# Performance work log

Hardware: AMD Instinct MI355X
Metric: run time of the kernel (lower is better)

Reference implementation:

```python
import jax, jax.numpy as jnp
import numpy as np

EPS = 1e-6
NUM_HEADS = 16  # config.num_attention_heads

def _rms(h, w):
    h32 = h.astype(jnp.float32)
    v = jnp.mean(h32 * h32, axis=-1, keepdims=True)
    return (w * h32 * jax.lax.rsqrt(v + EPS)).astype(h.dtype)

def _rope(q, k, pos):
    dh = q.shape[-1]
    inv = 1.0 / (10000.0 ** (jnp.arange(0, dh, 2, dtype=jnp.float32) / dh))
    ang = pos.astype(jnp.float32)[:, None] * inv[None, :]  # [n, dh/2]
    cos = jnp.concatenate([jnp.cos(ang), jnp.cos(ang)], -1)[None, None]  # [1,1,n,dh]
    sin = jnp.concatenate([jnp.sin(ang), jnp.sin(ang)], -1)[None, None]
    def rot(x):
        x1, x2 = x[..., :dh // 2], x[..., dh // 2:]
        return jnp.concatenate([-x2, x1], -1)
    return q * cos + rot(q) * sin, k * cos + rot(k) * sin

def _skip_causal_mask(N, block_size, len1, text_len):
    qi = jnp.arange(N)[:, None]
    ki = jnp.arange(N)[None, :]
    qb = (qi - text_len) // block_size
    kb = (ki - text_len) // block_size
    iq = qi >= text_len
    ik = ki >= text_len
    return (((ki < text_len) & (qi >= ki))
            | (iq & ik & (qb < len1) & (kb < len1) & (qb >= kb))
            | (iq & ik & (qb >= len1) & (kb < len1) & (qb - len1 > kb))
            | (iq & ik & (qb == kb)))

def _layer(x, position_ids, text_position_ids, qkv_w, qkv_b, proj_w, proj_b,
           qn_w, kn_w, ln1_w, ln2_w, gate_w, up_w, down_w,
           block_size, text_len, len1):
    B, N, C = x.shape
    H = NUM_HEADS
    Dh = C // H
    T = text_len
    Lc = len1 * block_size
    offs = [0, T, T + Lc]
    lens = [T, Lc, N - T - Lc]  # text / clean / noised segment lengths
    qs, ks, vs = [], [], []
    for i in range(3):
        seg = _rms(x[:, offs[i]:offs[i] + lens[i]], ln1_w[i])  # input layernorm
        qkv = seg @ qkv_w[i] + qkv_b[i]                        # [B,n,3C]
        qkv = qkv.reshape(B, lens[i], 3, H, Dh).transpose(2, 0, 3, 1, 4)
        qs.append(_rms(qkv[0], qn_w[i]))
        ks.append(_rms(qkv[1], kn_w[i]))
        vs.append(qkv[2])
    img_q = jnp.concatenate([qs[1], qs[2]], axis=2)
    img_k = jnp.concatenate([ks[1], ks[2]], axis=2)
    img_q, img_k = _rope(img_q, img_k, position_ids)
    txt_q, txt_k = _rope(qs[0], ks[0], text_position_ids)
    q = jnp.concatenate([txt_q, img_q], axis=2)
    k = jnp.concatenate([txt_k, img_k], axis=2)
    v = jnp.concatenate(vs, axis=2)
    scores = jnp.einsum('bhqd,bhkd->bhqk', q, k) / np.float32(np.sqrt(Dh))
    mask = _skip_causal_mask(N, block_size, len1, text_len)
    scores = jnp.where(mask, scores, jnp.finfo(scores.dtype).min)
    attn = jax.nn.softmax(scores, axis=-1)
    o = jnp.einsum('bhqk,bhkd->bhqd', attn, v)
    o = o.transpose(0, 2, 1, 3).reshape(B, N, C)
    o = jnp.concatenate([o[:, offs[i]:offs[i] + lens[i]] @ proj_w[i] + proj_b[i]
                         for i in range(3)], axis=1)
    h = x + o
    mlp = []
    for i in range(3):
        y = _rms(h[:, offs[i]:offs[i] + lens[i]], ln2_w[i])  # post-attn layernorm
        mlp.append((jax.nn.silu(y @ gate_w[i]) * (y @ up_w[i])) @ down_w[i])
    return h + jnp.concatenate(mlp, axis=1)

def setup_inputs():
    key = jax.random.key(0)
    ks = jax.random.split(key, 8)
    B, C, H, I = 2, 1024, 16, 4096
    block_size, text_len, len1, len2 = 128, 256, 4, 4
    N = text_len + (len1 + len2) * block_size  # 1280
    s = 0.02
    return {
        'x': jax.random.normal(ks[0], (B, N, C), jnp.float32),
        'position_ids': jnp.arange((len1 + len2) * block_size, dtype=jnp.int32),
        'text_position_ids': jnp.arange(text_len, dtype=jnp.int32),
        'qkv_w': jax.random.normal(ks[1], (3, C, 3 * C), jnp.float32) * s,
        'qkv_b': jnp.zeros((3, 3 * C), jnp.float32),
        'proj_w': jax.random.normal(ks[2], (3, C, C), jnp.float32) * s,
        'proj_b': jnp.zeros((3, C), jnp.float32),
        'qn_w': jnp.ones((3, C // H), jnp.float32),
        'kn_w': jnp.ones((3, C // H), jnp.float32),
        'ln1_w': jnp.ones((3, C), jnp.float32),
        'ln2_w': jnp.ones((3, C), jnp.float32),
        'gate_w': jax.random.normal(ks[3], (3, C, I), jnp.float32) * s,
        'up_w': jax.random.normal(ks[4], (3, C, I), jnp.float32) * s,
        'down_w': jax.random.normal(ks[5], (3, I, C), jnp.float32) * s,
        'block_size': block_size, 'text_len': text_len, 'len1': len1,
    }

def reference(x, position_ids, text_position_ids, qkv_w, qkv_b, proj_w, proj_b,
              qn_w, kn_w, ln1_w, ln2_w, gate_w, up_w, down_w,
              block_size, text_len, len1):
    return _layer(x, position_ids, text_position_ids, qkv_w, qkv_b, proj_w, proj_b,
                  qn_w, kn_w, ln1_w, ln2_w, gate_w, up_w, down_w,
                  block_size, text_len, len1)
```

## Files before the change

### kernel.cpp

```cpp
#include <hip/hip_runtime.h>
#include <math.h>

constexpr int Bb  = 2;
constexpr int Nn  = 1280;
constexpr int Cc  = 1024;
constexpr int Hh  = 16;
constexpr int DH  = 64;
constexpr int Ii  = 4096;
constexpr int Tt  = 256;
constexpr int BSz = 128;
constexpr int L1  = 4;
constexpr int Mrows = Bb * Nn;

typedef __attribute__((ext_vector_type(8))) short short8v;
typedef __attribute__((ext_vector_type(4))) float f32x4;

__device__ __forceinline__ int segof(int n) {
    return n < Tt ? 0 : (n < Tt + L1 * BSz ? 1 : 2);
}
__device__ __forceinline__ unsigned short f2bf(float f) {
    unsigned int u = __float_as_uint(f);
    u += 0x7fffu + ((u >> 16) & 1u);
    return (unsigned short)(u >> 16);
}
__device__ __forceinline__ float bf2f(unsigned short h) {
    return __uint_as_float(((unsigned int)h) << 16);
}

__device__ __forceinline__ int xcd_swz(int lin, int nwg) {
    int cpx = nwg >> 3;
    return (lin & 7) * cpx + (lin >> 3);
}

__device__ __forceinline__ void rms_dev(const float* __restrict__ in,
                                        const float* __restrict__ w,
                                        unsigned short* __restrict__ out,
                                        int row, float* sred) {
    int n   = row % Nn;
    int seg = segof(n);
    const float* x = in + (size_t)row * Cc;
    int t = threadIdx.x;
    float4 xv = reinterpret_cast<const float4*>(x)[t];
    float ss = xv.x * xv.x + xv.y * xv.y + xv.z * xv.z + xv.w * xv.w;
#pragma unroll
    for (int off = 32; off; off >>= 1) ss += __shfl_down(ss, off, 64);
    int lane = t & 63, wid = t >> 6;
    if (lane == 0) sred[wid] = ss;
    __syncthreads();
    if (t == 0) sred[4] = rsqrtf((sred[0] + sred[1] + sred[2] + sred[3]) * (1.0f / Cc) + 1e-6f);
    __syncthreads();
    float r = sred[4];
    float4 wv = reinterpret_cast<const float4*>(w + (size_t)seg * Cc)[t];
    ushort4 ov;
    ov.x = f2bf(wv.x * xv.x * r);
    ov.y = f2bf(wv.y * xv.y * r);
    ov.z = f2bf(wv.z * xv.z * r);
    ov.w = f2bf(wv.w * xv.w * r);
    *reinterpret_cast<ushort4*>(&out[(size_t)row * Cc + t * 4]) = ov;
}

__device__ __forceinline__ void pack_dev(const float* __restrict__ W,
                                         unsigned short* __restrict__ PB,
                                         int K, int Nd, size_t idx) {
    size_t cpseg = (size_t)K * Nd / 8;
    int s = (int)(idx / cpseg);
    size_t rm = idx % cpseg;
    int lane = (int)(rm & 63);
    int fr   = (int)((rm >> 6) & 7);
    size_t tile = rm >> 9;
    int nct = Nd >> 7;
    int cb = (int)(tile % nct);
    int kt = (int)(tile / nct);
    int col = cb * 128 + fr * 16 + (lane & 15);
    int k0  = kt * 32 + (lane >> 4) * 8;
    const float* src = W + ((size_t)s * K + k0) * Nd + col;
    unsigned short o[8];
#pragma unroll
    for (int j = 0; j < 8; j++) o[j] = f2bf(src[(size_t)j * Nd]);
    short8v v;
#pragma unroll
    for (int j = 0; j < 8; j++) v[j] = (short)o[j];
    *reinterpret_cast<short8v*>(&PB[idx * 8]) = v;
}

__global__ __launch_bounds__(256)
void rms_bf16(const float* __restrict__ in, const float* __restrict__ w,
              unsigned short* __restrict__ out) {
    __shared__ float sred[5];
    rms_dev(in, w, out, blockIdx.x, sred);
}

__global__ __launch_bounds__(256)
void pack_w(const float* __restrict__ W, unsigned short* __restrict__ PB,
            int K, int Nd) {
    pack_dev(W, PB, K, Nd, (size_t)blockIdx.x * 256 + threadIdx.x);
}

__global__ __launch_bounds__(256)
void fat1(const float* __restrict__ x, const float* __restrict__ ln1_w,
          unsigned short* __restrict__ xn,
          const float* __restrict__ qkv_w, unsigned short* __restrict__ qkv_p) {
    __shared__ float sred[5];
    int bid = blockIdx.x;
    if (bid < Mrows) {
        rms_dev(x, ln1_w, xn, bid, sred);
    } else {
        pack_dev(qkv_w, qkv_p, Cc, 3 * Cc, (size_t)(bid - Mrows) * 256 + threadIdx.x);
    }
}

__device__ __forceinline__ void attn_dev(
        const unsigned short* __restrict__ Qg, const unsigned short* __restrict__ Kg,
        const unsigned short* __restrict__ Vg, unsigned short* __restrict__ O,
        int qt, int bh,
        unsigned short* k_lds, unsigned short* vt_lds, unsigned short* p_base) {
    int b = bh >> 4, h = bh & 15;
    int tid = threadIdx.x, lane = tid & 63, wid = tid >> 6;
    int g = lane >> 4, c = lane & 15;

    const size_t headoff = (size_t)bh * Nn * DH;
    int q0 = qt * 64;
    bool qtext = q0 < Tt;
    int qb = qtext ? 0 : (q0 - Tt) / BSz;

    int qrow_frag = q0 + wid * 16 + c;
    short8v aq[2];
#pragma unroll
    for (int kb = 0; kb < 2; kb++)
        aq[kb] = *reinterpret_cast<const short8v*>(
            &Qg[headoff + (size_t)qrow_frag * DH + kb * 32 + g * 8]);

    unsigned short* pbuf = p_base + wid * 1024;

    f32x4 o_[4];
#pragma unroll
    for (int nb = 0; nb < 4; nb++) o_[nb] = (f32x4){0.f, 0.f, 0.f, 0.f};
    float m_[4] = {-3.4e38f, -3.4e38f, -3.4e38f, -3.4e38f};
    float l_[4] = {0.f, 0.f, 0.f, 0.f};

    int tr = tid >> 2, tc = tid & 3;

    for (int kt = 0; kt < Nn / 64; kt++) {
        int kbase = kt * 64;
        bool vis, diag = false;
        if (qtext) {
            vis = (kbase <= q0);
            diag = (kbase == q0);
        } else if (kbase < Tt) {
            vis = true;
        } else {
            int kb = (kbase - Tt) / BSz;
            vis = (qb < L1) ? (kb <= qb)
                            : ((kb < L1 && qb - L1 > kb) || kb == qb);
        }
        if (!vis) continue;

        __syncthreads();
        {
            const unsigned short* ks = &Kg[headoff + (size_t)(kbase + tr) * DH];
            const unsigned short* vs = &Vg[headoff + (size_t)(kbase + tr) * DH];
#pragma unroll
            for (int i = 0; i < 2; i++) {
                int ch = tc + i * 4;
                short8v kv = *reinterpret_cast<const short8v*>(ks + ch * 8);
                int byte = (tr * 128 + ch * 16) ^ ((tr & 7) << 4);
                *reinterpret_cast<short8v*>((char*)k_lds + byte) = kv;
                short8v vv = *reinterpret_cast<const short8v*>(vs + ch * 8);
#pragma unroll
                for (int j = 0; j < 8; j++) {
                    int dh = ch * 8 + j;
                    int vbyte = (dh * 128 + tr * 2) ^ ((dh & 7) << 4);
                    *reinterpret_cast<unsigned short*>((char*)vt_lds + vbyte) =
                        (unsigned short)vv[j];
                }
            }
        }
        __syncthreads();

        f32x4 s_[4];
#pragma unroll
        for (int nb = 0; nb < 4; nb++) s_[nb] = (f32x4){0.f, 0.f, 0.f, 0.f};
#pragma unroll
        for (int nb = 0; nb < 4; nb++) {
            int kil = nb * 16 + c;
#pragma unroll
            for (int kb = 0; kb < 2; kb++) {
                int byte = (kil * 128 + kb * 64 + g * 16) ^ ((kil & 7) << 4);
                short8v bk = *reinterpret_cast<short8v*>((char*)k_lds + byte);
                s_[nb] = __builtin_amdgcn_mfma_f32_16x16x32_bf16(aq[kb], bk, s_[nb], 0, 0, 0);
            }
        }
#pragma unroll
        for (int nb = 0; nb < 4; nb++) {
#pragma unroll
            for (int r = 0; r < 4; r++) {
                float sv = s_[nb][r] * 0.125f;
                if (diag) {
                    int qrl = wid * 16 + g * 4 + r;
                    int kcl = nb * 16 + c;
                    if (qrl < kcl) sv = -3.4e38f;
                }
                s_[nb][r] = sv;
            }
        }
#pragma unroll
        for (int r = 0; r < 4; r++) {
            float mx = fmaxf(fmaxf(s_[0][r], s_[1][r]), fmaxf(s_[2][r], s_[3][r]));
#pragma unroll
            for (int off = 1; off <= 8; off <<= 1)
                mx = fmaxf(mx, __shfl_xor(mx, off, 64));
            float mn = fmaxf(m_[r], mx);
            float es = __expf(m_[r] - mn);
            m_[r] = mn;
            float pv[4];
            float rs = 0.f;
#pragma unroll
            for (int nb = 0; nb < 4; nb++) {
                pv[nb] = __expf(s_[nb][r] - mn);
                rs += pv[nb];
            }
#pragma unroll
            for (int off = 1; off <= 8; off <<= 1)
                rs += __shfl_xor(rs, off, 64);
            l_[r] = l_[r] * es + rs;
#pragma unroll
            for (int nb = 0; nb < 4; nb++) o_[nb][r] *= es;
            int qrl = g * 4 + r;
            int swz = (qrl & 7) << 4;
#pragma unroll
            for (int nb = 0; nb < 4; nb++) {
                int byte = (qrl * 128 + (nb * 16 + c) * 2) ^ swz;
                *reinterpret_cast<unsigned short*>((char*)pbuf + byte) = f2bf(pv[nb]);
            }
        }
        short8v aP[2];
#pragma unroll
        for (int kb = 0; kb < 2; kb++) {
            int byte = (c * 128 + kb * 64 + g * 16) ^ ((c & 7) << 4);
            aP[kb] = *reinterpret_cast<short8v*>((char*)pbuf + byte);
        }
#pragma unroll
        for (int nb = 0; nb < 4; nb++) {
            int dh = nb * 16 + c;
#pragma unroll
            for (int kb = 0; kb < 2; kb++) {
                int byte = (dh * 128 + kb * 64 + g * 16) ^ ((dh & 7) << 4);
                short8v bv = *reinterpret_cast<short8v*>((char*)vt_lds + byte);
                o_[nb] = __builtin_amdgcn_mfma_f32_16x16x32_bf16(aP[kb], bv, o_[nb], 0, 0, 0);
            }
        }
    }

    float inv_[4];
#pragma unroll
    for (int r = 0; r < 4; r++) inv_[r] = 1.f / l_[r];
#pragma unroll
    for (int nb = 0; nb < 4; nb++) {
        int col = h * DH + nb * 16 + c;
#pragma unroll
        for (int r = 0; r < 4; r++) {
            int row = q0 + wid * 16 + g * 4 + r;
            O[((size_t)b * Nn + row) * Cc + col] = f2bf(o_[nb][r] * inv_[r]);
        }
    }
}

__global__ __launch_bounds__(256)
void fat2(const unsigned short* __restrict__ Qg, const unsigned short* __restrict__ Kg,
          const unsigned short* __restrict__ Vg, unsigned short* __restrict__ O,
          const float* __restrict__ proj_w, unsigned short* __restrict__ proj_p,
          const float* __restrict__ gate_w, unsigned short* __restrict__ gate_p,
          const float* __restrict__ up_w,   unsigned short* __restrict__ up_p) {
    __shared__ __align__(16) unsigned short k_lds[64 * 64];
    __shared__ __align__(16) unsigned short vt_lds[64 * 64];
    __shared__ __align__(16) unsigned short p_lds[4 * 16 * 64];
    int bid = blockIdx.x;
    if (bid < 640) {
        attn_dev(Qg, Kg, Vg, O, bid % 20, bid / 20, k_lds, vt_lds, p_lds);
        return;
    }
    bid -= 640;
    if (bid < 1536) {
        pack_dev(proj_w, proj_p, Cc, Cc, (size_t)bid * 256 + threadIdx.x);
        return;
    }
    bid -= 1536;
    if (bid < 6144) {
        pack_dev(gate_w, gate_p, Cc, Ii, (size_t)bid * 256 + threadIdx.x);
        return;
    }
    bid -= 6144;
    pack_dev(up_w, up_p, Cc, Ii, (size_t)bid * 256 + threadIdx.x);
}

template <int OUTMODE, bool BIAS, int NZ>
__global__ __launch_bounds__(256, 2)
void gemm128r(const unsigned short* __restrict__ A,
              const unsigned short* __restrict__ PB,
              const float* __restrict__ bias, void* __restrict__ outp,
              int K, int Nd) {
    __shared__ __align__(16) unsigned short lds[8192];
    int bx = blockIdx.x, by = blockIdx.y, bz = (NZ > 1) ? blockIdx.z : 0;
    {
        int gx = gridDim.x, gy = gridDim.y, gz = (NZ > 1) ? gridDim.z : 1;
        int lin = bx + gx * (by + gy * bz);
        int swz = xcd_swz(lin, gx * gy * gz);
        bx = swz % gx; swz /= gx;
        by = swz % gy; bz = swz / gy;
    }
    int rb = bx * 128, cb = by;
    int seg = segof(rb % Nn);
    int tid = threadIdx.x, lane = tid & 63, wid = tid >> 6;
    int wr = wid >> 1, wc = wid & 1;
    int g = lane >> 4, c_ = lane & 15;
    const int nct = Nd >> 7;
    const int Keff = K / NZ;
    const int nKt = Keff >> 5;
    const int kz = bz * Keff;
    const unsigned short* PBseg = PB + (size_t)seg * K * Nd;

    int mf0 = tid >> 6, lc0 = tid & 63;
    const unsigned short* pA0 =
        A + (size_t)(rb + mf0 * 16 + (lc0 & 15)) * K + kz + (lc0 >> 4) * 8;
    const unsigned short* pA1 = pA0 + (size_t)64 * K;
    const unsigned short* pB0 =
        PBseg + (((size_t)(kz >> 5) * nct + cb) * 8 + mf0) * 512 + (size_t)lc0 * 8;
    const unsigned short* pB1 = pB0 + 2048;
    const size_t bstep = (size_t)nct * 4096;

    f32x4 acc[4][4];
#pragma unroll
    for (int m = 0; m < 4; m++)
#pragma unroll
        for (int n = 0; n < 4; n++) acc[m][n] = (f32x4){0.f, 0.f, 0.f, 0.f};

    short8v av[2], bv[2];
    av[0] = *reinterpret_cast<const short8v*>(pA0);
    av[1] = *reinterpret_cast<const short8v*>(pA1);
    bv[0] = *reinterpret_cast<const short8v*>(pB0);
    bv[1] = *reinterpret_cast<const short8v*>(pB1);
    pA0 += 32; pA1 += 32; pB0 += bstep; pB1 += bstep;

    for (int kt = 0; kt < nKt; ++kt) {
        __syncthreads();
        *reinterpret_cast<short8v*>(&lds[(size_t)tid * 8]) = av[0];
        *reinterpret_cast<short8v*>(&lds[(size_t)(tid + 256) * 8]) = av[1];
        *reinterpret_cast<short8v*>(&lds[4096 + (size_t)tid * 8]) = bv[0];
        *reinterpret_cast<short8v*>(&lds[4096 + (size_t)(tid + 256) * 8]) = bv[1];
        __syncthreads();
        if (kt + 1 < nKt) {
            av[0] = *reinterpret_cast<const short8v*>(pA0);
            av[1] = *reinterpret_cast<const short8v*>(pA1);
            bv[0] = *reinterpret_cast<const short8v*>(pB0);
            bv[1] = *reinterpret_cast<const short8v*>(pB1);
            pA0 += 32; pA1 += 32; pB0 += bstep; pB1 += bstep;
        }
        short8v afr[4], bfr[4];
#pragma unroll
        for (int m = 0; m < 4; m++)
            afr[m] = *reinterpret_cast<short8v*>(&lds[((wr * 4 + m) * 64 + lane) * 8]);
#pragma unroll
        for (int n = 0; n < 4; n++)
            bfr[n] = *reinterpret_cast<short8v*>(&lds[4096 + ((wc * 4 + n) * 64 + lane) * 8]);
#pragma unroll
        for (int m = 0; m < 4; m++)
#pragma unroll
            for (int n = 0; n < 4; n++)
                acc[m][n] = __builtin_amdgcn_mfma_f32_16x16x32_bf16(
                    afr[m], bfr[n], acc[m][n], 0, 0, 0);
    }

    float* outf = (float*)outp;
    unsigned short* outh = (unsigned short*)outp;
    size_t zoff = (NZ > 1) ? (size_t)bz * Mrows * Nd : 0;
#pragma unroll
    for (int n = 0; n < 4; n++) {
        int col = cb * 128 + wc * 64 + n * 16 + c_;
        float bvv = BIAS ? bias[(size_t)seg * Nd + col] : 0.f;
#pragma unroll
        for (int m = 0; m < 4; m++) {
#pragma unroll
            for (int r = 0; r < 4; r++) {
                int row = rb + wr * 64 + m * 16 + g * 4 + r;
                float v = acc[m][n][r] + bvv;
                if (OUTMODE == 0) outf[zoff + (size_t)row * Nd + col] = v;
                else              outh[zoff + (size_t)row * Nd + col] = f2bf(v);
            }
        }
    }
}

__global__ __launch_bounds__(256)
void gemm_gu(const unsigned short* __restrict__ A,
             const unsigned short* __restrict__ PG,
             const unsigned short* __restrict__ PU,
             unsigned short* __restrict__ outp) {
    __shared__ __align__(16) unsigned short lds[10240];
    int bx = blockIdx.x, by = blockIdx.y;
    {
        int lin = bx + gridDim.x * by;
        int swz = xcd_swz(lin, gridDim.x * gridDim.y);
        bx = swz % gridDim.x; by = swz / gridDim.x;
    }
    int rb = bx * 64, cb = by;
    int seg = segof(rb % Nn);
    int tid = threadIdx.x, lane = tid & 63, wid = tid >> 6;
    int wr = wid >> 1, wc = wid & 1;
    int g = lane >> 4, c_ = lane & 15;
    const int nct = Ii >> 7;
    const unsigned short* PGseg = PG + (size_t)seg * Cc * Ii;
    const unsigned short* PUseg = PU + (size_t)seg * Cc * Ii;

    f32x4 accG[2][4], accU[2][4];
#pragma unroll
    for (int m = 0; m < 2; m++)
#pragma unroll
        for (int n = 0; n < 4; n++) {
            accG[m][n] = (f32x4){0.f, 0.f, 0.f, 0.f};
            accU[m][n] = (f32x4){0.f, 0.f, 0.f, 0.f};
        }

    int mf0 = tid >> 6, lc0 = tid & 63;
    const unsigned short* gA =
        &A[(size_t)(rb + mf0 * 16 + (lc0 & 15)) * Cc + (lc0 >> 4) * 8];
    short8v av, gv[2], uv[2];
    auto load_tile = [&](int kt) {
        av = *reinterpret_cast<const short8v*>(gA + kt * 32);
#pragma unroll
        for (int i = 0; i < 2; i++) {
            int c = tid + i * 256;
            int cf = c >> 6, lc = c & 63;
            size_t off = (((size_t)kt * nct + cb) * 8 + cf) * 64 * 8 + (size_t)lc * 8;
            gv[i] = *reinterpret_cast<const short8v*>(PGseg + off);
            uv[i] = *reinterpret_cast<const short8v*>(PUseg + off);
        }
    };

    const int nKt = Cc >> 5;
    load_tile(0);
    for (int kt = 0; kt < nKt; ++kt) {
        __syncthreads();
        *reinterpret_cast<short8v*>(&lds[(size_t)tid * 8]) = av;
#pragma unroll
        for (int i = 0; i < 2; i++) {
            *reinterpret_cast<short8v*>(&lds[2048 + (size_t)(tid + i * 256) * 8]) = gv[i];
            *reinterpret_cast<short8v*>(&lds[6144 + (size_t)(tid + i * 256) * 8]) = uv[i];
        }
        __syncthreads();
        if (kt + 1 < nKt) load_tile(kt + 1);
        short8v afr[2], gfr[4], ufr[4];
#pragma unroll
        for (int m = 0; m < 2; m++)
            afr[m] = *reinterpret_cast<short8v*>(&lds[((wr * 2 + m) * 64 + lane) * 8]);
#pragma unroll
        for (int n = 0; n < 4; n++) {
            gfr[n] = *reinterpret_cast<short8v*>(&lds[2048 + ((wc * 4 + n) * 64 + lane) * 8]);
            ufr[n] = *reinterpret_cast<short8v*>(&lds[6144 + ((wc * 4 + n) * 64 + lane) * 8]);
        }
#pragma unroll
        for (int m = 0; m < 2; m++)
#pragma unroll
            for (int n = 0; n < 4; n++) {
                accG[m][n] = __builtin_amdgcn_mfma_f32_16x16x32_bf16(
                    afr[m], gfr[n], accG[m][n], 0, 0, 0);
                accU[m][n] = __builtin_amdgcn_mfma_f32_16x16x32_bf16(
                    afr[m], ufr[n], accU[m][n], 0, 0, 0);
            }
    }

#pragma unroll
    for (int n = 0; n < 4; n++) {
        int col = cb * 128 + wc * 64 + n * 16 + c_;
#pragma unroll
        for (int m = 0; m < 2; m++) {
#pragma unroll
            for (int r = 0; r < 4; r++) {
                int row = rb + wr * 32 + m * 16 + g * 4 + r;
                float gval = accG[m][n][r], uval = accU[m][n][r];
                float t = gval / (1.f + __expf(-gval)) * uval;
                outp[(size_t)row * Ii + col] = f2bf(t);
            }
        }
    }
}

__global__ __launch_bounds__(256)
void combine_proj(const float* __restrict__ x, const float* __restrict__ bias,
                  const float* __restrict__ p, float* __restrict__ hb) {
    int i = blockIdx.x * 256 + threadIdx.x;
    int base = i * 4;
    int col = base % Cc;
    int n   = (base / Cc) % Nn;
    int seg = segof(n);
    float4 a = reinterpret_cast<const float4*>(x)[i];
    float4 b = *reinterpret_cast<const float4*>(&bias[(size_t)seg * Cc + col]);
    float4 p0 = reinterpret_cast<const float4*>(p)[i];
    float4 p1 = reinterpret_cast<const float4*>(p)[i + Mrows * Cc / 4];
    float4 r;
    r.x = a.x + b.x + p0.x + p1.x;
    r.y = a.y + b.y + p0.y + p1.y;
    r.z = a.z + b.z + p0.z + p1.z;
    r.w = a.w + b.w + p0.w + p1.w;
    reinterpret_cast<float4*>(hb)[i] = r;
}

__global__ __launch_bounds__(256)
void combine_down4(const unsigned short* __restrict__ p,
                   float* __restrict__ out) {
    int i = blockIdx.x * 256 + threadIdx.x;
    float4 a = reinterpret_cast<const float4*>(out)[i];
#pragma unroll
    for (int z = 0; z < 4; z++) {
        ushort4 u = *reinterpret_cast<const ushort4*>(&p[(size_t)z * Mrows * Cc + i * 4]);
        a.x += bf2f(u.x); a.y += bf2f(u.y); a.z += bf2f(u.z); a.w += bf2f(u.w);
    }
    reinterpret_cast<float4*>(out)[i] = a;
}

__global__ __launch_bounds__(256)
void split_rope(const unsigned short* __restrict__ qkv,
                const float* __restrict__ qn_w, const float* __restrict__ kn_w,
                const int* __restrict__ pos_ids, const int* __restrict__ tpos_ids,
                unsigned short* __restrict__ Q, unsigned short* __restrict__ K,
                unsigned short* __restrict__ V) {
    int row = blockIdx.x;
    int b = row / Nn, n = row % Nn;
    int seg = segof(n);
    int lane = threadIdx.x & 63, wid = threadIdx.x >> 6;
    int pos = (n < Tt) ? tpos_ids[n] : pos_ids[n - Tt];
    int j = lane & 31;
    float ang = (float)pos * exp2f(-(float)j * (13.287712379549449f / 32.f));
    float cv = cosf(ang), sv = sinf(ang);
    float qw = qn_w[seg * DH + lane], kw = kn_w[seg * DH + lane];
    for (int h = wid; h < Hh; h += 4) {
        const unsigned short* base = qkv + (size_t)row * (3 * Cc) + h * DH + lane;
        float q = bf2f(base[0]), k = bf2f(base[Cc]), v = bf2f(base[2 * Cc]);
        float qs = q * q, ks = k * k;
#pragma unroll
        for (int off = 32; off; off >>= 1) {
            qs += __shfl_xor(qs, off, 64);
            ks += __shfl_xor(ks, off, 64);
        }
        q = q * rsqrtf(qs * (1.f / DH) + 1e-6f) * qw;
        k = k * rsqrtf(ks * (1.f / DH) + 1e-6f) * kw;
        float qp = __shfl_xor(q, 32, 64);
        float kp = __shfl_xor(k, 32, 64);
        float qo = q * cv + ((lane < 32) ? -qp * sv : qp * sv);
        float ko = k * cv + ((lane < 32) ? -kp * sv : kp * sv);
        size_t oidx = ((size_t)(b * Hh + h) * Nn + n) * DH + lane;
        Q[oidx] = f2bf(qo);
        K[oidx] = f2bf(ko);
        V[oidx] = f2bf(v);
    }
}

extern "C" void kernel_launch(void* const* d_in, const int* in_sizes, int n_in,
                              void* d_out, int out_size, void* d_ws, size_t ws_size,
                              hipStream_t stream) {
    const float* x        = (const float*)d_in[0];
    const int*   pos_ids  = (const int*)d_in[1];
    const int*   tpos_ids = (const int*)d_in[2];
    const float* qkv_w    = (const float*)d_in[3];
    const float* qkv_b    = (const float*)d_in[4];
    const float* proj_w   = (const float*)d_in[5];
    const float* proj_b   = (const float*)d_in[6];
    const float* qn_w     = (const float*)d_in[7];
    const float* kn_w     = (const float*)d_in[8];
    const float* ln1_w    = (const float*)d_in[9];
    const float* ln2_w    = (const float*)d_in[10];
    const float* gate_w   = (const float*)d_in[11];
    const float* up_w     = (const float*)d_in[12];
    const float* down_w   = (const float*)d_in[13];
    float* out = (float*)d_out;
    char*  wsb = (char*)d_ws;

    unsigned short* WA  = (unsigned short*)(wsb);
    unsigned short* WB  = (unsigned short*)(wsb + 25165824);
    unsigned short* Tb  = (unsigned short*)(wsb + 50331648);
    unsigned short* P3  = (unsigned short*)(wsb + 71303168);
    unsigned short* P4  = (unsigned short*)(wsb + 76546048);
    unsigned short* Qbf = Tb;
    unsigned short* Kbf = Tb + 2621440;
    unsigned short* Vbf = Tb + 5242880;

    fat1<<<Mrows + 4608, 256, 0, stream>>>(x, ln1_w, P3, qkv_w, WA);
    gemm128r<1, true, 1><<<dim3(Mrows / 128, 24), 256, 0, stream>>>(
        P3, WA, qkv_b, WB, Cc, 3 * Cc);
    split_rope<<<Mrows, 256, 0, stream>>>(WB, qn_w, kn_w, pos_ids, tpos_ids,
                                          Qbf, Kbf, Vbf);
    fat2<<<640 + 1536 + 6144 + 6144, 256, 0, stream>>>(
        Qbf, Kbf, Vbf, P3, proj_w, P4, gate_w, WA, up_w, WB);
    gemm128r<0, false, 2><<<dim3(Mrows / 128, 8, 2), 256, 0, stream>>>(
        P3, P4, nullptr, (float*)Tb, Cc, Cc);
    combine_proj<<<Mrows * Cc / 1024, 256, 0, stream>>>(x, proj_b, (float*)Tb, out);
    rms_bf16<<<Mrows, 256, 0, stream>>>(out, ln2_w, P3);
    gemm_gu<<<dim3(Mrows / 64, 32), 256, 0, stream>>>(P3, WA, WB, Tb);
    pack_w<<<6144, 256, 0, stream>>>(down_w, WA, Ii, Cc);
    gemm128r<1, false, 4><<<dim3(Mrows / 128, 8, 4), 256, 0, stream>>>(
        Tb, WA, nullptr, WB, Ii, Cc);
    combine_down4<<<Mrows * Cc / 1024, 256, 0, stream>>>(WB, out);
}
```

Before: 249.0 us.

## Fuse proj combine with post-attention RMSNorm and retile gate/up warp layout

The projection-residual combine and the second RMSNorm become one per-row kernel. It writes the fp32 residual and the normalized bf16 activations in a single pass, which saves a kernel launch and a full re-read of the hidden state. The gate/up GEMM also changes its per-wave tiling from 2x4 to 4x1-row-block by 2-col fragments, so every wave reads all four A fragments and only two B fragment pairs. That shifts the LDS read mix and may change bank-conflict behaviour.

```diff
diff --git a/kernel.cpp b/kernel.cpp
--- a/kernel.cpp
+++ b/kernel.cpp
@@ -84,13 +84,6 @@
 }
 
 __global__ __launch_bounds__(256)
-void rms_bf16(const float* __restrict__ in, const float* __restrict__ w,
-              unsigned short* __restrict__ out) {
-    __shared__ float sred[5];
-    rms_dev(in, w, out, blockIdx.x, sred);
-}
-
-__global__ __launch_bounds__(256)
 void pack_w(const float* __restrict__ W, unsigned short* __restrict__ PB,
             int K, int Nd) {
     pack_dev(W, PB, K, Nd, (size_t)blockIdx.x * 256 + threadIdx.x);
@@ -405,17 +398,16 @@
     int rb = bx * 64, cb = by;
     int seg = segof(rb % Nn);
     int tid = threadIdx.x, lane = tid & 63, wid = tid >> 6;
-    int wr = wid >> 1, wc = wid & 1;
     int g = lane >> 4, c_ = lane & 15;
     const int nct = Ii >> 7;
     const unsigned short* PGseg = PG + (size_t)seg * Cc * Ii;
     const unsigned short* PUseg = PU + (size_t)seg * Cc * Ii;
 
-    f32x4 accG[2][4], accU[2][4];
-#pragma unroll
-    for (int m = 0; m < 2; m++)
-#pragma unroll
-        for (int n = 0; n < 4; n++) {
+    f32x4 accG[4][2], accU[4][2];
+#pragma unroll
+    for (int m = 0; m < 4; m++)
+#pragma unroll
+        for (int n = 0; n < 2; n++) {
             accG[m][n] = (f32x4){0.f, 0.f, 0.f, 0.f};
             accU[m][n] = (f32x4){0.f, 0.f, 0.f, 0.f};
         }
@@ -448,19 +440,19 @@
         }
         __syncthreads();
         if (kt + 1 < nKt) load_tile(kt + 1);
-        short8v afr[2], gfr[4], ufr[4];
-#pragma unroll
-        for (int m = 0; m < 2; m++)
-            afr[m] = *reinterpret_cast<short8v*>(&lds[((wr * 2 + m) * 64 + lane) * 8]);
-#pragma unroll
-        for (int n = 0; n < 4; n++) {
-            gfr[n] = *reinterpret_cast<short8v*>(&lds[2048 + ((wc * 4 + n) * 64 + lane) * 8]);
-            ufr[n] = *reinterpret_cast<short8v*>(&lds[6144 + ((wc * 4 + n) * 64 + lane) * 8]);
-        }
-#pragma unroll
-        for (int m = 0; m < 2; m++)
-#pragma unroll
-            for (int n = 0; n < 4; n++) {
+        short8v afr[4], gfr[2], ufr[2];
+#pragma unroll
+        for (int m = 0; m < 4; m++)
+            afr[m] = *reinterpret_cast<short8v*>(&lds[((m) * 64 + lane) * 8]);
+#pragma unroll
+        for (int n = 0; n < 2; n++) {
+            gfr[n] = *reinterpret_cast<short8v*>(&lds[2048 + ((wid * 2 + n) * 64 + lane) * 8]);
+            ufr[n] = *reinterpret_cast<short8v*>(&lds[6144 + ((wid * 2 + n) * 64 + lane) * 8]);
+        }
+#pragma unroll
+        for (int m = 0; m < 4; m++)
+#pragma unroll
+            for (int n = 0; n < 2; n++) {
                 accG[m][n] = __builtin_amdgcn_mfma_f32_16x16x32_bf16(
                     afr[m], gfr[n], accG[m][n], 0, 0, 0);
                 accU[m][n] = __builtin_amdgcn_mfma_f32_16x16x32_bf16(
@@ -469,13 +461,13 @@
     }
 
 #pragma unroll
-    for (int n = 0; n < 4; n++) {
-        int col = cb * 128 + wc * 64 + n * 16 + c_;
-#pragma unroll
-        for (int m = 0; m < 2; m++) {
+    for (int n = 0; n < 2; n++) {
+        int col = cb * 128 + (wid * 2 + n) * 16 + c_;
+#pragma unroll
+        for (int m = 0; m < 4; m++) {
 #pragma unroll
             for (int r = 0; r < 4; r++) {
-                int row = rb + wr * 32 + m * 16 + g * 4 + r;
+                int row = rb + m * 16 + g * 4 + r;
                 float gval = accG[m][n][r], uval = accU[m][n][r];
                 float t = gval / (1.f + __expf(-gval)) * uval;
                 outp[(size_t)row * Ii + col] = f2bf(t);
@@ -485,23 +477,41 @@
 }
 
 __global__ __launch_bounds__(256)
-void combine_proj(const float* __restrict__ x, const float* __restrict__ bias,
-                  const float* __restrict__ p, float* __restrict__ hb) {
-    int i = blockIdx.x * 256 + threadIdx.x;
-    int base = i * 4;
-    int col = base % Cc;
-    int n   = (base / Cc) % Nn;
+void combine_rms(const float* __restrict__ x, const float* __restrict__ bias,
+                 const float* __restrict__ p, const float* __restrict__ ln2_w,
+                 float* __restrict__ out, unsigned short* __restrict__ y) {
+    int row = blockIdx.x;
+    int n   = row % Nn;
     int seg = segof(n);
-    float4 a = reinterpret_cast<const float4*>(x)[i];
-    float4 b = *reinterpret_cast<const float4*>(&bias[(size_t)seg * Cc + col]);
+    int t   = threadIdx.x;
+    size_t i = (size_t)row * 256 + t;
+    float4 a  = reinterpret_cast<const float4*>(x)[i];
+    float4 b  = *reinterpret_cast<const float4*>(&bias[(size_t)seg * Cc + t * 4]);
     float4 p0 = reinterpret_cast<const float4*>(p)[i];
     float4 p1 = reinterpret_cast<const float4*>(p)[i + Mrows * Cc / 4];
-    float4 r;
-    r.x = a.x + b.x + p0.x + p1.x;
-    r.y = a.y + b.y + p0.y + p1.y;
-    r.z = a.z + b.z + p0.z + p1.z;
-    r.w = a.w + b.w + p0.w + p1.w;
-    reinterpret_cast<float4*>(hb)[i] = r;
+    float4 h;
+    h.x = a.x + b.x + p0.x + p1.x;
+    h.y = a.y + b.y + p0.y + p1.y;
+    h.z = a.z + b.z + p0.z + p1.z;
+    h.w = a.w + b.w + p0.w + p1.w;
+    reinterpret_cast<float4*>(out)[i] = h;
+    float ss = h.x * h.x + h.y * h.y + h.z * h.z + h.w * h.w;
+#pragma unroll
+    for (int off = 32; off; off >>= 1) ss += __shfl_down(ss, off, 64);
+    __shared__ float sred[5];
+    int lane = t & 63, wid = t >> 6;
+    if (lane == 0) sred[wid] = ss;
+    __syncthreads();
+    if (t == 0) sred[4] = rsqrtf((sred[0] + sred[1] + sred[2] + sred[3]) * (1.0f / Cc) + 1e-6f);
+    __syncthreads();
+    float r = sred[4];
+    float4 wv = reinterpret_cast<const float4*>(ln2_w + (size_t)seg * Cc)[t];
+    ushort4 ov;
+    ov.x = f2bf(wv.x * h.x * r);
+    ov.y = f2bf(wv.y * h.y * r);
+    ov.z = f2bf(wv.z * h.z * r);
+    ov.w = f2bf(wv.w * h.w * r);
+    *reinterpret_cast<ushort4*>(&y[(size_t)row * Cc + t * 4]) = ov;
 }
 
 __global__ __launch_bounds__(256)
@@ -592,8 +602,7 @@
         Qbf, Kbf, Vbf, P3, proj_w, P4, gate_w, WA, up_w, WB);
     gemm128r<0, false, 2><<<dim3(Mrows / 128, 8, 2), 256, 0, stream>>>(
         P3, P4, nullptr, (float*)Tb, Cc, Cc);
-    combine_proj<<<Mrows * Cc / 1024, 256, 0, stream>>>(x, proj_b, (float*)Tb, out);
-    rms_bf16<<<Mrows, 256, 0, stream>>>(out, ln2_w, P3);
+    combine_rms<<<Mrows, 256, 0, stream>>>(x, proj_b, (float*)Tb, ln2_w, out, P3);
     gemm_gu<<<dim3(Mrows / 64, 32), 256, 0, stream>>>(P3, WA, WB, Tb);
     pack_w<<<6144, 256, 0, stream>>>(down_w, WA, Ii, Cc);
     gemm128r<1, false, 4><<<dim3(Mrows / 128, 8, 4), 256, 0, stream>>>(
```

Measured after the change: 247.2 us. About the same (-0.7%).
